# Kernel optimization log

Hardware: AMD Instinct MI355X
Metric: run time of the kernel (lower is better)

Reference implementation:

```python
import jax, jax.numpy as jnp
import numpy as np

D_MODEL = 768
NUM_HEADS = 12
D_K = D_MODEL // NUM_HEADS


def setup_inputs() -> dict:
    key = jax.random.key(0)
    ks = jax.random.split(key, 11)
    B, L = 1, 4096
    s = 1.0 / np.sqrt(D_MODEL)
    return {
        "q": jax.random.normal(ks[0], (B, L, D_MODEL), jnp.float32),
        "k": jax.random.normal(ks[1], (B, L, D_MODEL), jnp.float32),
        "v": jax.random.normal(ks[2], (B, L, D_MODEL), jnp.float32),
        "Wq": jax.random.normal(ks[3], (D_MODEL, D_MODEL), jnp.float32) * s,
        "bq": jax.random.normal(ks[4], (D_MODEL,), jnp.float32) * s,
        "Wk": jax.random.normal(ks[5], (D_MODEL, D_MODEL), jnp.float32) * s,
        "bk": jax.random.normal(ks[6], (D_MODEL,), jnp.float32) * s,
        "Wv": jax.random.normal(ks[7], (D_MODEL, D_MODEL), jnp.float32) * s,
        "bv": jax.random.normal(ks[8], (D_MODEL,), jnp.float32) * s,
        "Wo": jax.random.normal(ks[9], (D_MODEL, D_MODEL), jnp.float32) * s,
        "bo": jax.random.normal(ks[10], (D_MODEL,), jnp.float32) * s,
    }


def reference(q, k, v, Wq, bq, Wk, bk, Wv, bv, Wo, bo):
    B, L, _ = q.shape
    # linear projections (torch Linear: x @ W.T + b)
    qp = q @ Wq.T + bq
    kp = k @ Wk.T + bk
    vp = v @ Wv.T + bv
    # split heads: (B, H, L, d_k)
    def split(x):
        return x.reshape(B, L, NUM_HEADS, D_K).transpose(0, 2, 1, 3)
    qh, kh, vh = split(qp), split(kp), split(vp)
    scale = 1.0 / jnp.sqrt(jnp.asarray(D_K, qh.dtype))
    scores = jnp.einsum("bhqd,bhkd->bhqk", qh, kh) * scale  # (B,H,L,L)
    weights = jax.nn.softmax(scores, axis=-1)
    out = jnp.einsum("bhqk,bhkd->bhqd", weights, vh)
    out = out.transpose(0, 2, 1, 3).reshape(B, L, D_MODEL)
    return out @ Wo.T + bo
```

## Files before the change

### kernel.cpp

```cpp
#include <hip/hip_runtime.h>
#include <stdint.h>
#include <math.h>

#define L_SEQ  4096
#define DMODEL 768
#define NHEADS 12
#define DKH    64
#define QSCALE 0.18033688011112042f

typedef _Float16 f16;
typedef __attribute__((ext_vector_type(8))) _Float16 half8;
typedef __attribute__((ext_vector_type(4))) _Float16 half4;
typedef __attribute__((ext_vector_type(4))) float f32x4;

#define MFMA16(a, b, c) __builtin_amdgcn_mfma_f32_16x16x32_f16(a, b, c, 0, 0, 0)

#define NE ((size_t)L_SEQ * DMODEL)
#define WE ((size_t)DMODEL * DMODEL)

__global__ __launch_bounds__(256)
void cvt_all(const float* __restrict__ q, const float* __restrict__ k,
             const float* __restrict__ v, const float* __restrict__ Wq,
             const float* __restrict__ Wk, const float* __restrict__ Wv,
             const float* __restrict__ Wo, f16* __restrict__ x16,
             f16* __restrict__ w16)
{
  const size_t NE4 = NE / 4, WE4 = WE / 4;
  size_t i = (size_t)blockIdx.x * 256 + threadIdx.x;
  const float* srcs[7] = {q, k, v, Wq, Wk, Wv, Wo};
  f16* dsts[7] = {x16, x16 + NE, x16 + 2 * NE,
                  w16, w16 + WE, w16 + 2 * WE, w16 + 3 * WE};
  const size_t sz4[7] = {NE4, NE4, NE4, WE4, WE4, WE4, WE4};
  int r = 0; size_t off = i;
  while (off >= sz4[r]) { off -= sz4[r]; ++r; }
  float4 f = reinterpret_cast<const float4*>(srcs[r])[off];
  half4 h; h[0] = (f16)f.x; h[1] = (f16)f.y; h[2] = (f16)f.z; h[3] = (f16)f.w;
  reinterpret_cast<half4*>(dsts[r])[off] = h;
}

__global__ __launch_bounds__(256)
void qkv_gemm(const f16* __restrict__ x16, const f16* __restrict__ w16,
              const float* __restrict__ bq, const float* __restrict__ bk,
              const float* __restrict__ bv,
              f16* __restrict__ Qp, f16* __restrict__ Kp, f16* __restrict__ VpT)
{
  __shared__ f16 As[128][40];
  __shared__ f16 Bs[64][40];
  const int tid  = threadIdx.x;
  const int lane = tid & 63, wid = tid >> 6;
  const int lq   = lane & 15, quad = lane >> 4;
  const int wm   = (wid & 1) * 64, wn = (wid >> 1) * 32;
  const int m0   = blockIdx.y * 128;
  const int widx = blockIdx.x / 12;
  const int n0   = (blockIdx.x % 12) * 64;
  const f16* X = x16 + (size_t)widx * NE;
  const f16* W = w16 + (size_t)widx * WE;
  const float* Bv = (widx == 0) ? bq : (widx == 1) ? bk : bv;

  const int arow = tid >> 1, aseg = (tid & 1) * 16;
  const int brow = tid >> 2, bseg = (tid & 3) * 8;
  const f16* aptr = X + (size_t)(m0 + arow) * DMODEL + aseg;
  const f16* bptr = W + (size_t)(n0 + brow) * DMODEL + bseg;

  half8 a0 = *reinterpret_cast<const half8*>(aptr);
  half8 a1 = *reinterpret_cast<const half8*>(aptr + 8);
  half8 b0 = *reinterpret_cast<const half8*>(bptr);

  f32x4 acc[4][2] = {};

  for (int k0 = 0; k0 < DMODEL; k0 += 32) {
    *reinterpret_cast<half8*>(&As[arow][aseg])     = a0;
    *reinterpret_cast<half8*>(&As[arow][aseg + 8]) = a1;
    *reinterpret_cast<half8*>(&Bs[brow][bseg])     = b0;
    __syncthreads();

    if (k0 + 32 < DMODEL) {
      a0 = *reinterpret_cast<const half8*>(aptr + k0 + 32);
      a1 = *reinterpret_cast<const half8*>(aptr + k0 + 40);
      b0 = *reinterpret_cast<const half8*>(bptr + k0 + 32);
    }

    half8 bf[2];
#pragma unroll
    for (int nf = 0; nf < 2; ++nf)
      bf[nf] = *reinterpret_cast<half8*>(&Bs[wn + nf * 16 + lq][quad * 8]);
#pragma unroll
    for (int mf = 0; mf < 4; ++mf) {
      half8 af = *reinterpret_cast<half8*>(&As[wm + mf * 16 + lq][quad * 8]);
#pragma unroll
      for (int nf = 0; nf < 2; ++nf)
        acc[mf][nf] = MFMA16(af, bf[nf], acc[mf][nf]);
    }
    __syncthreads();
  }

#pragma unroll
  for (int nf = 0; nf < 2; ++nf) {
    const int col  = n0 + wn + nf * 16 + lq;
    const float bias = Bv[col];
#pragma unroll
    for (int mf = 0; mf < 4; ++mf) {
      const int rowb = m0 + wm + mf * 16 + quad * 4;
      if (widx == 2) {
        half4 o4;
#pragma unroll
        for (int r = 0; r < 4; ++r) o4[r] = (f16)(acc[mf][nf][r] + bias);
        *reinterpret_cast<half4*>(VpT + (size_t)col * L_SEQ + rowb) = o4;
      } else if (widx == 0) {
#pragma unroll
        for (int r = 0; r < 4; ++r)
          Qp[(size_t)(rowb + r) * DMODEL + col] = (f16)((acc[mf][nf][r] + bias) * QSCALE);
      } else {
#pragma unroll
        for (int r = 0; r < 4; ++r)
          Kp[(size_t)(rowb + r) * DMODEL + col] = (f16)(acc[mf][nf][r] + bias);
      }
    }
  }
}

__global__ __launch_bounds__(256)
void attn_mfma3(const f16* __restrict__ Qp, const f16* __restrict__ Kp,
                const f16* __restrict__ VpT, f16* __restrict__ AO)
{
  const int h  = blockIdx.x;
  const int q0 = blockIdx.y * 64;
  const int tid  = threadIdx.x;
  const int lane = tid & 63, wid = tid >> 6;
  const int lq   = lane & 15, quad = lane >> 4;

  __shared__ f16 Ks[64][72];
  __shared__ f16 Vt[64][72];
  __shared__ f16 Ps[4][16][72];

  half8 qf[2];
#pragma unroll
  for (int ks = 0; ks < 2; ++ks)
    qf[ks] = *reinterpret_cast<const half8*>(
        Qp + (size_t)(q0 + wid * 16 + lq) * DMODEL + h * DKH + ks * 32 + quad * 8);

  half8 ones;
#pragma unroll
  for (int j = 0; j < 8; ++j) ones[j] = (f16)1.0f;

  f32x4 oacc[4] = {};
  f32x4 lacc = {};

  const int srow = tid >> 2, sseg = (tid & 3) * 16;
  const f16* kbase = Kp  + (size_t)srow * DMODEL + h * DKH + sseg;
  const f16* vbase = VpT + (size_t)(h * DKH + srow) * L_SEQ + sseg;

  half8 k0 = *reinterpret_cast<const half8*>(kbase);
  half8 k1 = *reinterpret_cast<const half8*>(kbase + 8);
  half8 v0 = *reinterpret_cast<const half8*>(vbase);
  half8 v1 = *reinterpret_cast<const half8*>(vbase + 8);

  for (int kt = 0; kt < L_SEQ; kt += 64) {
    *reinterpret_cast<half8*>(&Ks[srow][sseg])     = k0;
    *reinterpret_cast<half8*>(&Ks[srow][sseg + 8]) = k1;
    *reinterpret_cast<half8*>(&Vt[srow][sseg])     = v0;
    *reinterpret_cast<half8*>(&Vt[srow][sseg + 8]) = v1;
    __syncthreads();

    if (kt + 64 < L_SEQ) {
      const f16* kn = kbase + (size_t)(kt + 64) * DMODEL;
      const f16* vn = vbase + (kt + 64);
      k0 = *reinterpret_cast<const half8*>(kn);
      k1 = *reinterpret_cast<const half8*>(kn + 8);
      v0 = *reinterpret_cast<const half8*>(vn);
      v1 = *reinterpret_cast<const half8*>(vn + 8);
    }

    f32x4 s[4] = {};
#pragma unroll
    for (int ks = 0; ks < 2; ++ks)
#pragma unroll
      for (int kf = 0; kf < 4; ++kf) {
        half8 kfrag = *reinterpret_cast<half8*>(&Ks[kf * 16 + lq][ks * 32 + quad * 8]);
        s[kf] = MFMA16(kfrag, qf[ks], s[kf]);
      }

#pragma unroll
    for (int kf = 0; kf < 4; ++kf) {
      half4 p4;
#pragma unroll
      for (int r = 0; r < 4; ++r) p4[r] = (f16)exp2f(s[kf][r]);
      *reinterpret_cast<half4*>(&Ps[wid][lq][kf * 16 + quad * 4]) = p4;
    }

#pragma unroll
    for (int ks = 0; ks < 2; ++ks) {
      half8 pf = *reinterpret_cast<half8*>(&Ps[wid][lq][ks * 32 + quad * 8]);
      lacc = MFMA16(ones, pf, lacc);
#pragma unroll
      for (int df = 0; df < 4; ++df) {
        half8 vf = *reinterpret_cast<half8*>(&Vt[df * 16 + lq][ks * 32 + quad * 8]);
        oacc[df] = MFMA16(vf, pf, oacc[df]);
      }
    }
    __syncthreads();
  }

  const float inv = 1.0f / lacc[0];
  const int qrow = q0 + wid * 16 + lq;
#pragma unroll
  for (int df = 0; df < 4; ++df) {
    half4 o4;
#pragma unroll
    for (int r = 0; r < 4; ++r) o4[r] = (f16)(oacc[df][r] * inv);
    *reinterpret_cast<half4*>(AO + (size_t)qrow * DMODEL + h * DKH + df * 16 + quad * 4) = o4;
  }
}

__global__ __launch_bounds__(256)
void out_gemm(const f16* __restrict__ A, const f16* __restrict__ W,
              const float* __restrict__ Bv, float* __restrict__ O)
{
  __shared__ f16 As[64][72];
  __shared__ f16 Bs[64][72];
  const int tid  = threadIdx.x;
  const int lane = tid & 63, wid = tid >> 6;
  const int lq   = lane & 15, quad = lane >> 4;
  const int wm   = (wid & 1) * 32, wn = (wid >> 1) * 32;
  const int m0   = blockIdx.y * 64, n0 = blockIdx.x * 64;

  const int row = tid >> 2, seg = (tid & 3) * 16;
  const f16* aptr = A + (size_t)(m0 + row) * DMODEL + seg;
  const f16* bptr = W + (size_t)(n0 + row) * DMODEL + seg;

  half8 a0 = *reinterpret_cast<const half8*>(aptr);
  half8 a1 = *reinterpret_cast<const half8*>(aptr + 8);
  half8 b0 = *reinterpret_cast<const half8*>(bptr);
  half8 b1 = *reinterpret_cast<const half8*>(bptr + 8);

  f32x4 acc[2][2] = {};

  for (int k0 = 0; k0 < DMODEL; k0 += 64) {
    *reinterpret_cast<half8*>(&As[row][seg])     = a0;
    *reinterpret_cast<half8*>(&As[row][seg + 8]) = a1;
    *reinterpret_cast<half8*>(&Bs[row][seg])     = b0;
    *reinterpret_cast<half8*>(&Bs[row][seg + 8]) = b1;
    __syncthreads();

    if (k0 + 64 < DMODEL) {
      a0 = *reinterpret_cast<const half8*>(aptr + k0 + 64);
      a1 = *reinterpret_cast<const half8*>(aptr + k0 + 72);
      b0 = *reinterpret_cast<const half8*>(bptr + k0 + 64);
      b1 = *reinterpret_cast<const half8*>(bptr + k0 + 72);
    }

#pragma unroll
    for (int ks = 0; ks < 2; ++ks) {
      half8 bf[2];
#pragma unroll
      for (int nf = 0; nf < 2; ++nf)
        bf[nf] = *reinterpret_cast<half8*>(&Bs[wn + nf * 16 + lq][ks * 32 + quad * 8]);
#pragma unroll
      for (int mf = 0; mf < 2; ++mf) {
        half8 af = *reinterpret_cast<half8*>(&As[wm + mf * 16 + lq][ks * 32 + quad * 8]);
#pragma unroll
        for (int nf = 0; nf < 2; ++nf)
          acc[mf][nf] = MFMA16(af, bf[nf], acc[mf][nf]);
      }
    }
    __syncthreads();
  }

#pragma unroll
  for (int nf = 0; nf < 2; ++nf) {
    const int col = n0 + wn + nf * 16 + lq;
    const float bias = Bv[col];
#pragma unroll
    for (int mf = 0; mf < 2; ++mf) {
      const int rowb = m0 + wm + mf * 16 + quad * 4;
#pragma unroll
      for (int r = 0; r < 4; ++r)
        O[(size_t)(rowb + r) * DMODEL + col] = acc[mf][nf][r] + bias;
    }
  }
}

extern "C" void kernel_launch(void* const* d_in, const int* in_sizes, int n_in,
                              void* d_out, int out_size, void* d_ws, size_t ws_size,
                              hipStream_t stream) {
  const float* q  = (const float*)d_in[0];
  const float* k  = (const float*)d_in[1];
  const float* v  = (const float*)d_in[2];
  const float* Wq = (const float*)d_in[3];
  const float* bq = (const float*)d_in[4];
  const float* Wk = (const float*)d_in[5];
  const float* bk = (const float*)d_in[6];
  const float* Wv = (const float*)d_in[7];
  const float* bv = (const float*)d_in[8];
  const float* Wo = (const float*)d_in[9];
  const float* bo = (const float*)d_in[10];
  float* out = (float*)d_out;

  f16* x16 = (f16*)d_ws;
  f16* w16 = x16 + 3 * NE;
  f16* Qp  = w16 + 4 * WE;
  f16* Kp  = Qp + NE;
  f16* VpT = Kp + NE;
  f16* AO  = VpT + NE;

  const int ncvt = (int)((3 * (NE / 4) + 4 * (WE / 4)) / 256);
  cvt_all<<<ncvt, 256, 0, stream>>>(q, k, v, Wq, Wk, Wv, Wo, x16, w16);

  dim3 gqkv(36, L_SEQ / 128);
  qkv_gemm<<<gqkv, 256, 0, stream>>>(x16, w16, bq, bk, bv, Qp, Kp, VpT);

  dim3 gattn(NHEADS, L_SEQ / 64);
  attn_mfma3<<<gattn, 256, 0, stream>>>(Qp, Kp, VpT, AO);

  dim3 gout(DMODEL / 64, L_SEQ / 64);
  out_gemm<<<gout, 256, 0, stream>>>(AO, w16 + 3 * WE, bo, out);
}
```

Before: 255.4 us.

## Rewrite attention with 32x32 MFMA, register-resident P, and split-K combine

```diff
diff --git a/kernel.cpp b/kernel.cpp
--- a/kernel.cpp
+++ b/kernel.cpp
@@ -12,11 +12,18 @@
 typedef __attribute__((ext_vector_type(8))) _Float16 half8;
 typedef __attribute__((ext_vector_type(4))) _Float16 half4;
 typedef __attribute__((ext_vector_type(4))) float f32x4;
+typedef __attribute__((ext_vector_type(16))) float f32x16;
+typedef __attribute__((ext_vector_type(4))) unsigned int uint4v;
 
 #define MFMA16(a, b, c) __builtin_amdgcn_mfma_f32_16x16x32_f16(a, b, c, 0, 0, 0)
+#define MFMA32(a, b, c) __builtin_amdgcn_mfma_f32_32x32x16_f16(a, b, c, 0, 0, 0)
 
 #define NE ((size_t)L_SEQ * DMODEL)
 #define WE ((size_t)DMODEL * DMODEL)
+
+static __device__ __forceinline__ unsigned int pack2(float a, float b) {
+  return __builtin_bit_cast(unsigned int, __builtin_amdgcn_cvt_pkrtz(a, b));
+}
 
 __global__ __launch_bounds__(256)
 void cvt_all(const float* __restrict__ q, const float* __restrict__ k,
@@ -119,32 +126,32 @@
   }
 }
 
-__global__ __launch_bounds__(256)
-void attn_mfma3(const f16* __restrict__ Qp, const f16* __restrict__ Kp,
+__global__ __launch_bounds__(256, 3)
+void attn_mfma4(const f16* __restrict__ Qp, const f16* __restrict__ Kp,
                 const f16* __restrict__ VpT, f16* __restrict__ AO)
 {
   const int h  = blockIdx.x;
   const int q0 = blockIdx.y * 64;
   const int tid  = threadIdx.x;
   const int lane = tid & 63, wid = tid >> 6;
-  const int lq   = lane & 15, quad = lane >> 4;
-
-  __shared__ f16 Ks[64][72];
-  __shared__ f16 Vt[64][72];
-  __shared__ f16 Ps[4][16][72];
-
-  half8 qf[2];
-#pragma unroll
-  for (int ks = 0; ks < 2; ++ks)
-    qf[ks] = *reinterpret_cast<const half8*>(
-        Qp + (size_t)(q0 + wid * 16 + lq) * DMODEL + h * DKH + ks * 32 + quad * 8);
-
-  half8 ones;
-#pragma unroll
-  for (int j = 0; j < 8; ++j) ones[j] = (f16)1.0f;
-
-  f32x4 oacc[4] = {};
-  f32x4 lacc = {};
+  const int l31  = lane & 31, hc = lane >> 5;
+  const int qh   = wid & 1, kh = wid >> 1;
+
+  __shared__ __align__(16) char smem[25088];
+  f16 (*Ks)[72] = (f16 (*)[72])smem;
+  f16 (*Vt)[72] = (f16 (*)[72])(smem + 9216);
+  float* Of  = (float*)smem;
+  float* lf  = (float*)(smem + 16384);
+  f16*   Of16 = (f16*)(smem + 16640);
+
+  half8 qf[4];
+#pragma unroll
+  for (int st = 0; st < 4; ++st)
+    qf[st] = *reinterpret_cast<const half8*>(
+        Qp + (size_t)(q0 + qh * 32 + l31) * DMODEL + h * DKH + st * 16 + hc * 8);
+
+  f32x16 oacc[2] = {};
+  float lsum = 0.0f;
 
   const int srow = tid >> 2, sseg = (tid & 3) * 16;
   const f16* kbase = Kp  + (size_t)srow * DMODEL + h * DKH + sseg;
@@ -171,45 +178,79 @@
       v1 = *reinterpret_cast<const half8*>(vn + 8);
     }
 
-    f32x4 s[4] = {};
-#pragma unroll
-    for (int ks = 0; ks < 2; ++ks)
-#pragma unroll
-      for (int kf = 0; kf < 4; ++kf) {
-        half8 kfrag = *reinterpret_cast<half8*>(&Ks[kf * 16 + lq][ks * 32 + quad * 8]);
-        s[kf] = MFMA16(kfrag, qf[ks], s[kf]);
-      }
-
-#pragma unroll
-    for (int kf = 0; kf < 4; ++kf) {
-      half4 p4;
-#pragma unroll
-      for (int r = 0; r < 4; ++r) p4[r] = (f16)exp2f(s[kf][r]);
-      *reinterpret_cast<half4*>(&Ps[wid][lq][kf * 16 + quad * 4]) = p4;
-    }
-
-#pragma unroll
-    for (int ks = 0; ks < 2; ++ks) {
-      half8 pf = *reinterpret_cast<half8*>(&Ps[wid][lq][ks * 32 + quad * 8]);
-      lacc = MFMA16(ones, pf, lacc);
-#pragma unroll
-      for (int df = 0; df < 4; ++df) {
-        half8 vf = *reinterpret_cast<half8*>(&Vt[df * 16 + lq][ks * 32 + quad * 8]);
-        oacc[df] = MFMA16(vf, pf, oacc[df]);
-      }
-    }
-    __syncthreads();
-  }
-
-  const float inv = 1.0f / lacc[0];
-  const int qrow = q0 + wid * 16 + lq;
-#pragma unroll
-  for (int df = 0; df < 4; ++df) {
-    half4 o4;
-#pragma unroll
-    for (int r = 0; r < 4; ++r) o4[r] = (f16)(oacc[df][r] * inv);
-    *reinterpret_cast<half4*>(AO + (size_t)qrow * DMODEL + h * DKH + df * 16 + quad * 4) = o4;
-  }
+    f32x16 s = {};
+#pragma unroll
+    for (int st = 0; st < 4; ++st) {
+      half8 kf = *reinterpret_cast<half8*>(&Ks[kh * 32 + l31][st * 16 + hc * 8]);
+      s = MFMA32(kf, qf[st], s);
+    }
+
+    unsigned int pk[8];
+#pragma unroll
+    for (int i = 0; i < 8; ++i) {
+      float p0 = exp2f(s[2 * i]);
+      float p1 = exp2f(s[2 * i + 1]);
+      lsum += p0 + p1;
+      pk[i] = pack2(p0, p1);
+    }
+
+    unsigned int recv[4];
+#pragma unroll
+    for (int j = 0; j < 4; ++j) {
+      unsigned int sv = hc ? pk[(j & 1) + 4 * (j >> 1)]
+                           : pk[2 + (j & 1) + 4 * (j >> 1)];
+      recv[j] = (unsigned int)__shfl_xor((int)sv, 32);
+    }
+
+#pragma unroll
+    for (int st = 0; st < 2; ++st) {
+      uint4v pw;
+#pragma unroll
+      for (int t = 0; t < 4; ++t) {
+        unsigned int h0v = (t < 2) ? pk[(t & 1) + 4 * st] : recv[2 * st + (t & 1)];
+        unsigned int h1v = (t < 2) ? recv[2 * st + (t & 1)] : pk[(t & 1) + 4 * st + 2];
+        pw[t] = hc ? h1v : h0v;
+      }
+      half8 pf = __builtin_bit_cast(half8, pw);
+#pragma unroll
+      for (int a = 0; a < 2; ++a) {
+        half8 vf = *reinterpret_cast<half8*>(&Vt[a * 32 + l31][kh * 32 + st * 16 + hc * 8]);
+        oacc[a] = MFMA32(vf, pf, oacc[a]);
+      }
+    }
+    __syncthreads();
+  }
+
+  float lw = lsum + __shfl_xor(lsum, 32);
+
+  if (kh == 0) {
+#pragma unroll
+    for (int a = 0; a < 2; ++a)
+#pragma unroll
+      for (int r = 0; r < 16; ++r) {
+        int d = a * 32 + (r & 3) + 8 * (r >> 2) + 4 * hc;
+        Of[((qh * 64) + d) * 32 + l31] = oacc[a][r];
+      }
+    if (lane < 32) lf[qh * 32 + l31] = lw;
+  }
+  __syncthreads();
+  if (kh == 1) {
+    const float inv = 1.0f / (lf[qh * 32 + l31] + lw);
+#pragma unroll
+    for (int a = 0; a < 2; ++a)
+#pragma unroll
+      for (int r = 0; r < 16; ++r) {
+        int d = a * 32 + (r & 3) + 8 * (r >> 2) + 4 * hc;
+        float val = (Of[((qh * 64) + d) * 32 + l31] + oacc[a][r]) * inv;
+        Of16[(qh * 32 + l31) * 64 + d] = (f16)val;
+      }
+  }
+  __syncthreads();
+
+  *reinterpret_cast<half8*>(AO + (size_t)(q0 + srow) * DMODEL + h * DKH + sseg) =
+      *reinterpret_cast<half8*>(&Of16[srow * 64 + sseg]);
+  *reinterpret_cast<half8*>(AO + (size_t)(q0 + srow) * DMODEL + h * DKH + sseg + 8) =
+      *reinterpret_cast<half8*>(&Of16[srow * 64 + sseg + 8]);
 }
 
 __global__ __launch_bounds__(256)
@@ -310,7 +351,7 @@
   qkv_gemm<<<gqkv, 256, 0, stream>>>(x16, w16, bq, bk, bv, Qp, Kp, VpT);
 
   dim3 gattn(NHEADS, L_SEQ / 64);
-  attn_mfma3<<<gattn, 256, 0, stream>>>(Qp, Kp, VpT, AO);
+  attn_mfma4<<<gattn, 256, 0, stream>>>(Qp, Kp, VpT, AO);
 
   dim3 gout(DMODEL / 64, L_SEQ / 64);
   out_gemm<<<gout, 256, 0, stream>>>(AO, w16 + 3 * WE, bo, out);
```

Measured after the change: 246.2 us. 1.04x faster.
